# Kernel tuning notes

Hardware: AMD Instinct MI355X
Metric: run time of the kernel (lower is better)

## Reference

```python
import jax, jax.numpy as jnp
import numpy as np

B, K, P, T = 4096, 128, 64, 4

def setup_inputs() -> dict:
    key = jax.random.key(0)
    ks = jax.random.split(key, 9)
    s = lambda k, shp: jax.random.normal(k, shp, dtype=jnp.float32) * 0.1
    return {
        "x": jax.random.normal(ks[0], (B, K, 1), dtype=jnp.float32),
        "w": jax.random.normal(ks[1], (B, K, 1), dtype=jnp.float32),
        "W1": s(ks[2], (P, 1)),   # theta_1: 1 -> p
        "W2": s(ks[3], (P, P)),   # theta_2: p -> p
        "W3": s(ks[4], (P, P)),   # theta_3: p -> p
        "W4": s(ks[5], (P, 1)),   # theta_4: 1 -> p
        "W5": s(ks[6], (1, 2 * P)),  # theta_5: 2p -> 1
        "W6": s(ks[7], (P, P)),   # theta_6: p -> p
        "W7": s(ks[8], (P, P)),   # theta_7: p -> p
    }


def reference(x, w, W1, W2, W3, W4, W5, W6, W7):
    # x, w: (B, K, 1). torch Linear(in,out,bias=False): y = v @ W.T, W: (out,in)
    b, k, _ = x.shape
    p = W1.shape[0]
    # per-node feature messages (invariant across T iterations in original code)
    tmsg = jax.nn.relu(jnp.einsum('bki,pi->bkp', w, W4))   # relu(theta_4(w_k)), (B,K,p)
    sum_t = tmsg.sum(axis=1, keepdims=True)                # (B,1,p)
    xmsg = jnp.einsum('bki,pi->bkp', x, W1)                # theta_1(x_k), (B,K,p)
    mu = jnp.zeros((b, k, p), dtype=x.dtype)
    for _ in range(T):
        sum_mu = mu.sum(axis=1, keepdims=True)             # (B,1,p)
        mu = jax.nn.relu(
            xmsg
            + jnp.einsum('bkp,qp->bkq', sum_mu - mu, W2)   # theta_2(sum_mu - mu_k)
            + jnp.einsum('bkp,qp->bkq', sum_t - tmsg, W3)  # theta_3(sum_t - t_k)
        )
    pooled = jax.nn.relu(jnp.einsum('bp,qp->bq', mu.sum(axis=1), W6))  # (B,p)
    local = jnp.einsum('bkp,qp->bkq', mu, W7)                           # (B,K,p)
    # theta_5(concat(relu(theta_6(pool)), theta_7(mu_k))); split W5 = [W5a | W5b]
    W5a, W5b = W5[:, :p], W5[:, p:]
    q = jnp.einsum('bp,op->bo', pooled, W5a)[:, None, :] + jnp.einsum('bkp,op->bko', local, W5b)
    return q  # (B, K, 1)
```

## Files before the change

kernel.cpp:

```cpp
#include <hip/hip_runtime.h>

typedef __bf16 bf16;
typedef __bf16 bf16x4 __attribute__((ext_vector_type(4)));
typedef __bf16 bf16x8 __attribute__((ext_vector_type(8)));
typedef float  f32x4  __attribute__((ext_vector_type(4)));

#define MFMA16(a, b, c) __builtin_amdgcn_mfma_f32_16x16x32_bf16((a), (b), (c), 0, 0, 0)

__global__ __launch_bounds__(64, 2)
void qnet_kernel(const float* __restrict__ Xg, const float* __restrict__ Wg,
                 const float* __restrict__ W1g, const float* __restrict__ W2g,
                 const float* __restrict__ W3g, const float* __restrict__ W4g,
                 const float* __restrict__ W5g, const float* __restrict__ W6g,
                 const float* __restrict__ W7g, float* __restrict__ Outg)
{
    __shared__ __align__(16) bf16 muS[128 * 64];
    __shared__ __align__(16) float uS[64];
    __shared__ __align__(16) float smS[64];

    const int lane = threadIdx.x;
    const int b    = blockIdx.x;
    const int l15  = lane & 15;
    const int quad = lane >> 4;
    const int sw   = l15 & 7;

    float xv0 = Xg[b * 128 + lane], xv1 = Xg[b * 128 + 64 + lane];
    float wv0 = Wg[b * 128 + lane], wv1 = Wg[b * 128 + 64 + lane];

    float Ap = fmaxf(wv0, 0.f) + fmaxf(wv1, 0.f);
    float Bn = fmaxf(-wv0, 0.f) + fmaxf(-wv1, 0.f);
#pragma unroll
    for (int m = 1; m < 64; m <<= 1) { Ap += __shfl_xor(Ap, m); Bn += __shfl_xor(Bn, m); }

    float sp = 0.f, sm = 0.f;
#pragma unroll
    for (int c = 0; c < 16; ++c) {
        f32x4 w4 = *(const f32x4*)&W4g[c * 4];
        f32x4 w3 = *(const f32x4*)&W3g[lane * 64 + c * 4];
#pragma unroll
        for (int e = 0; e < 4; ++e) {
            sp += fmaxf(w4[e], 0.f) * w3[e];
            sm += fmaxf(-w4[e], 0.f) * w3[e];
        }
    }
    float w1C[16], v3pC[16], v3mC[16];
#pragma unroll
    for (int qt = 0; qt < 4; ++qt) {
        f32x4 w1v = *(const f32x4*)&W1g[qt * 16 + quad * 4];
#pragma unroll
        for (int e = 0; e < 4; ++e) {
            const int q = qt * 16 + quad * 4 + e;
            v3pC[qt * 4 + e] = __shfl(sp, q);
            v3mC[qt * 4 + e] = __shfl(sm, q);
            w1C[qt * 4 + e]  = w1v[e];
        }
    }

    {
        float u = 0.f;
#pragma unroll
        for (int c = 0; c < 16; ++c) {
            f32x4 w5v = *(const f32x4*)&W5g[64 + c * 4];
#pragma unroll
            for (int e = 0; e < 4; ++e) u += w5v[e] * W7g[(c * 4 + e) * 64 + lane];
        }
        uS[lane] = u;
    }

    bf16x8 w2h[4][2];
#pragma unroll
    for (int qt = 0; qt < 4; ++qt)
#pragma unroll
        for (int s = 0; s < 2; ++s) {
            const float* src = &W2g[(qt * 16 + l15) * 64 + s * 32 + quad * 8];
            f32x4 f0 = *(const f32x4*)src;
            f32x4 f1 = *(const f32x4*)(src + 4);
            bf16x8 h;
#pragma unroll
            for (int e = 0; e < 4; ++e) { h[e] = (bf16)f0[e]; h[4 + e] = (bf16)f1[e]; }
            w2h[qt][s] = h;
        }

    float smv[16];
#pragma unroll
    for (int i = 0; i < 16; ++i) smv[i] = 0.f;
#pragma unroll
    for (int kt = 0; kt < 8; ++kt) {
        const int src = (kt & 3) * 16 + l15;
        float xs_ = __shfl((kt < 4) ? xv0 : xv1, src);
        float ws_ = __shfl((kt < 4) ? wv0 : wv1, src);
        float ap_ = Ap - fmaxf(ws_, 0.f);
        float bn_ = Bn - fmaxf(-ws_, 0.f);
        const int row = (kt * 16 + l15) * 64;
#pragma unroll
        for (int qt = 0; qt < 4; ++qt) {
            bf16x4 h;
#pragma unroll
            for (int e = 0; e < 4; ++e) {
                float t = fmaf(xs_, w1C[qt * 4 + e],
                          fmaf(ap_, v3pC[qt * 4 + e], bn_ * v3mC[qt * 4 + e]));
                float v = fmaxf(t, 0.f);
                smv[qt * 4 + e] += v;
                h[e] = (bf16)v;
            }
            *(bf16x4*)&muS[row + ((2 * qt + (quad >> 1)) ^ sw) * 8 + 4 * (quad & 1)] = h;
        }
    }

    const f32x4 zero4 = {0.f, 0.f, 0.f, 0.f};
    for (int it = 0; it < 3; ++it) {
#pragma unroll
        for (int m = 1; m <= 8; m <<= 1)
#pragma unroll
            for (int i = 0; i < 16; ++i) smv[i] += __shfl_xor(smv[i], m);
        if (l15 == 0) {
#pragma unroll
            for (int qt = 0; qt < 4; ++qt) {
                f32x4 v = {smv[qt * 4], smv[qt * 4 + 1], smv[qt * 4 + 2], smv[qt * 4 + 3]};
                *(f32x4*)&smS[qt * 16 + quad * 4] = v;
            }
        }
        bf16x8 bs0, bs1;
        {
            f32x4 pA = *(const f32x4*)&smS[quad * 8];
            f32x4 pB = *(const f32x4*)&smS[quad * 8 + 4];
#pragma unroll
            for (int e = 0; e < 4; ++e) {
                bf16 h = (bf16)pA[e];
                bs0[e] = (l15 == 0) ? h : ((l15 == 1) ? (bf16)(pA[e] - (float)h) : (bf16)0.f);
                bf16 g = (bf16)pB[e];
                bs0[4 + e] = (l15 == 0) ? g : ((l15 == 1) ? (bf16)(pB[e] - (float)g) : (bf16)0.f);
            }
            pA = *(const f32x4*)&smS[32 + quad * 8];
            pB = *(const f32x4*)&smS[32 + quad * 8 + 4];
#pragma unroll
            for (int e = 0; e < 4; ++e) {
                bf16 h = (bf16)pA[e];
                bs1[e] = (l15 == 0) ? h : ((l15 == 1) ? (bf16)(pA[e] - (float)h) : (bf16)0.f);
                bf16 g = (bf16)pB[e];
                bs1[4 + e] = (l15 == 0) ? g : ((l15 == 1) ? (bf16)(pB[e] - (float)g) : (bf16)0.f);
            }
        }
        f32x4 s2q[4];
#pragma unroll
        for (int qt = 0; qt < 4; ++qt) {
            f32x4 a = MFMA16(w2h[qt][0], bs0, zero4);
            a = MFMA16(w2h[qt][1], bs1, a);
#pragma unroll
            for (int e = 0; e < 4; ++e)
                s2q[qt][e] = __shfl(a[e], quad * 16) + __shfl(a[e], quad * 16 + 1);
        }

#pragma unroll
        for (int i = 0; i < 16; ++i) smv[i] = 0.f;
#pragma unroll
        for (int kt = 0; kt < 8; ++kt) {
            const int src = (kt & 3) * 16 + l15;
            float xs_ = __shfl((kt < 4) ? xv0 : xv1, src);
            float ws_ = __shfl((kt < 4) ? wv0 : wv1, src);
            float ap_ = Ap - fmaxf(ws_, 0.f);
            float bn_ = Bn - fmaxf(-ws_, 0.f);
            const int row = (kt * 16 + l15) * 64;
            bf16x8 m0 = *(const bf16x8*)&muS[row + ((quad) ^ sw) * 8];
            bf16x8 m1 = *(const bf16x8*)&muS[row + ((4 + quad) ^ sw) * 8];
#pragma unroll
            for (int qt = 0; qt < 4; ++qt) {
                f32x4 a = MFMA16(w2h[qt][0], m0, zero4);
                a = MFMA16(w2h[qt][1], m1, a);
                bf16x4 h;
#pragma unroll
                for (int e = 0; e < 4; ++e) {
                    float t = fmaf(xs_, w1C[qt * 4 + e], s2q[qt][e]);
                    t = fmaf(ap_, v3pC[qt * 4 + e], t);
                    t = fmaf(bn_, v3mC[qt * 4 + e], t);
                    float v = fmaxf(t - a[e], 0.f);
                    smv[qt * 4 + e] += v;
                    h[e] = (bf16)v;
                }
                *(bf16x4*)&muS[row + ((2 * qt + (quad >> 1)) ^ sw) * 8 + 4 * (quad & 1)] = h;
            }
        }
    }

#pragma unroll
    for (int m = 1; m <= 8; m <<= 1)
#pragma unroll
        for (int i = 0; i < 16; ++i) smv[i] += __shfl_xor(smv[i], m);
    if (l15 == 0) {
#pragma unroll
        for (int qt = 0; qt < 4; ++qt) {
            f32x4 v = {smv[qt * 4], smv[qt * 4 + 1], smv[qt * 4 + 2], smv[qt * 4 + 3]};
            *(f32x4*)&smS[qt * 16 + quad * 4] = v;
        }
    }

    float pl = 0.f;
#pragma unroll
    for (int c = 0; c < 16; ++c) {
        f32x4 sv = *(const f32x4*)&smS[c * 4];
        f32x4 w6 = *(const f32x4*)&W6g[lane * 64 + c * 4];
#pragma unroll
        for (int e = 0; e < 4; ++e) pl = fmaf(sv[e], w6[e], pl);
    }
    float qa = fmaxf(pl, 0.f) * W5g[lane];
#pragma unroll
    for (int m = 1; m < 64; m <<= 1) qa += __shfl_xor(qa, m);

    f32x4 uf[2][2];
#pragma unroll
    for (int s = 0; s < 2; ++s) {
        uf[s][0] = *(const f32x4*)&uS[s * 32 + quad * 8];
        uf[s][1] = *(const f32x4*)&uS[s * 32 + quad * 8 + 4];
    }

    float res[8];
#pragma unroll
    for (int kt = 0; kt < 8; ++kt) {
        const int row = (kt * 16 + l15) * 64;
        bf16x8 m0 = *(const bf16x8*)&muS[row + ((quad) ^ sw) * 8];
        bf16x8 m1 = *(const bf16x8*)&muS[row + ((4 + quad) ^ sw) * 8];
        float r = 0.f;
#pragma unroll
        for (int j = 0; j < 4; ++j) {
            r = fmaf((float)m0[j],     uf[0][0][j], r);
            r = fmaf((float)m0[4 + j], uf[0][1][j], r);
            r = fmaf((float)m1[j],     uf[1][0][j], r);
            r = fmaf((float)m1[4 + j], uf[1][1][j], r);
        }
        r += __shfl_xor(r, 16); r += __shfl_xor(r, 32);
        res[kt] = r;
    }
    float rA0 = (quad & 1) ? res[1] : res[0];
    float rA1 = (quad & 1) ? res[3] : res[2];
    float rA  = (quad & 2) ? rA1 : rA0;
    float rB0 = (quad & 1) ? res[5] : res[4];
    float rB1 = (quad & 1) ? res[7] : res[6];
    float rB  = (quad & 2) ? rB1 : rB0;
    Outg[b * 128 + lane]      = qa + rA;
    Outg[b * 128 + 64 + lane] = qa + rB;
}

extern "C" void kernel_launch(void* const* d_in, const int* in_sizes, int n_in,
                              void* d_out, int out_size, void* d_ws, size_t ws_size,
                              hipStream_t stream) {
    (void)n_in; (void)d_ws; (void)ws_size; (void)out_size;
    const int B = in_sizes[0] >> 7;
    qnet_kernel<<<B, 64, 0, stream>>>(
        (const float*)d_in[0], (const float*)d_in[1], (const float*)d_in[2],
        (const float*)d_in[3], (const float*)d_in[4], (const float*)d_in[5],
        (const float*)d_in[6], (const float*)d_in[7], (const float*)d_in[8],
        (float*)d_out);
}
```

Before: 125.0 us.

## Keep last three mu row tiles in registers to shrink LDS footprint

Only the first five 16-row tiles of mu stay in shared memory. The remaining three tiles are written to a single scratch tile and read back into per-lane bf16x8 registers, which serve as the MFMA B operand in later iterations and in the final readout. This cuts LDS per block from 16KB to about 12KB, intended to let more blocks share a CU. The cost is more VGPRs per lane and an extra LDS round-trip through the scratch tile, which could lower occupancy or add latency.

```diff
diff --git a/kernel.cpp b/kernel.cpp
--- a/kernel.cpp
+++ b/kernel.cpp
@@ -6,6 +6,8 @@
 typedef float  f32x4  __attribute__((ext_vector_type(4)));
 
 #define MFMA16(a, b, c) __builtin_amdgcn_mfma_f32_16x16x32_bf16((a), (b), (c), 0, 0, 0)
+
+#define LDS_KT 5
 
 __global__ __launch_bounds__(64, 2)
 void qnet_kernel(const float* __restrict__ Xg, const float* __restrict__ Wg,
@@ -14,9 +16,10 @@
                  const float* __restrict__ W5g, const float* __restrict__ W6g,
                  const float* __restrict__ W7g, float* __restrict__ Outg)
 {
-    __shared__ __align__(16) bf16 muS[128 * 64];
+    __shared__ __align__(16) bf16 muS[(LDS_KT + 1) * 16 * 64];
     __shared__ __align__(16) float uS[64];
     __shared__ __align__(16) float smS[64];
+    const int SCR = LDS_KT * 16 * 64;
 
     const int lane = threadIdx.x;
     const int b    = blockIdx.x;
@@ -80,6 +83,8 @@
             for (int e = 0; e < 4; ++e) { h[e] = (bf16)f0[e]; h[4 + e] = (bf16)f1[e]; }
             w2h[qt][s] = h;
         }
+
+    bf16x8 mr0[8 - LDS_KT], mr1[8 - LDS_KT];
 
     float smv[16];
 #pragma unroll
@@ -91,7 +96,7 @@
         float ws_ = __shfl((kt < 4) ? wv0 : wv1, src);
         float ap_ = Ap - fmaxf(ws_, 0.f);
         float bn_ = Bn - fmaxf(-ws_, 0.f);
-        const int row = (kt * 16 + l15) * 64;
+        const int row = (kt < LDS_KT) ? (kt * 16 + l15) * 64 : (SCR + l15 * 64);
 #pragma unroll
         for (int qt = 0; qt < 4; ++qt) {
             bf16x4 h;
@@ -105,6 +110,10 @@
             }
             *(bf16x4*)&muS[row + ((2 * qt + (quad >> 1)) ^ sw) * 8 + 4 * (quad & 1)] = h;
         }
+        if (kt >= LDS_KT) {
+            mr0[kt - LDS_KT] = *(const bf16x8*)&muS[row + ((quad) ^ sw) * 8];
+            mr1[kt - LDS_KT] = *(const bf16x8*)&muS[row + ((4 + quad) ^ sw) * 8];
+        }
     }
 
     const f32x4 zero4 = {0.f, 0.f, 0.f, 0.f};
@@ -160,9 +169,15 @@
             float ws_ = __shfl((kt < 4) ? wv0 : wv1, src);
             float ap_ = Ap - fmaxf(ws_, 0.f);
             float bn_ = Bn - fmaxf(-ws_, 0.f);
-            const int row = (kt * 16 + l15) * 64;
-            bf16x8 m0 = *(const bf16x8*)&muS[row + ((quad) ^ sw) * 8];
-            bf16x8 m1 = *(const bf16x8*)&muS[row + ((4 + quad) ^ sw) * 8];
+            const int row = (kt < LDS_KT) ? (kt * 16 + l15) * 64 : (SCR + l15 * 64);
+            bf16x8 m0, m1;
+            if (kt < LDS_KT) {
+                m0 = *(const bf16x8*)&muS[row + ((quad) ^ sw) * 8];
+                m1 = *(const bf16x8*)&muS[row + ((4 + quad) ^ sw) * 8];
+            } else {
+                m0 = mr0[kt - LDS_KT];
+                m1 = mr1[kt - LDS_KT];
+            }
 #pragma unroll
             for (int qt = 0; qt < 4; ++qt) {
                 f32x4 a = MFMA16(w2h[qt][0], m0, zero4);
@@ -179,6 +194,10 @@
                 }
                 *(bf16x4*)&muS[row + ((2 * qt + (quad >> 1)) ^ sw) * 8 + 4 * (quad & 1)] = h;
             }
+            if (kt >= LDS_KT) {
+                mr0[kt - LDS_KT] = *(const bf16x8*)&muS[row + ((quad) ^ sw) * 8];
+                mr1[kt - LDS_KT] = *(const bf16x8*)&muS[row + ((4 + quad) ^ sw) * 8];
+            }
         }
     }
 
@@ -216,9 +235,15 @@
     float res[8];
 #pragma unroll
     for (int kt = 0; kt < 8; ++kt) {
-        const int row = (kt * 16 + l15) * 64;
-        bf16x8 m0 = *(const bf16x8*)&muS[row + ((quad) ^ sw) * 8];
-        bf16x8 m1 = *(const bf16x8*)&muS[row + ((4 + quad) ^ sw) * 8];
+        bf16x8 m0, m1;
+        if (kt < LDS_KT) {
+            const int row = (kt * 16 + l15) * 64;
+            m0 = *(const bf16x8*)&muS[row + ((quad) ^ sw) * 8];
+            m1 = *(const bf16x8*)&muS[row + ((4 + quad) ^ sw) * 8];
+        } else {
+            m0 = mr0[kt - LDS_KT];
+            m1 = mr1[kt - LDS_KT];
+        }
         float r = 0.f;
 #pragma unroll
         for (int j = 0; j < 4; ++j) {
```

After: 127.4 us. About the same (+1.9%).
